# Performance work log

Hardware: AMD Instinct MI355X
Metric: run time of the kernel (lower is better)

## Reference

```python
import jax, jax.numpy as jnp
import numpy as np

DIM = 192
HEADS = 6
HIDDEN = 384  # int(DIM * 2.0)


def _ln(x, w, b):
    # WithBias LayerNorm over channel dim (torch normalizes last dim of b,(hw),c)
    mu = jnp.mean(x, axis=1, keepdims=True)
    var = jnp.var(x, axis=1, keepdims=True)
    return (x - mu) / jnp.sqrt(var + 1e-5) * w[None, :, None, None] + b[None, :, None, None]


def _conv1x1(x, w):  # w: [O, I, 1, 1]
    return jnp.einsum('bihw,oi->bohw', x, w[:, :, 0, 0])


def _dwconv3(x, w):  # depthwise 3x3, w: [C, 1, 3, 3]
    return jax.lax.conv_general_dilated(
        x, w, window_strides=(1, 1), padding=((1, 1), (1, 1)),
        feature_group_count=x.shape[1],
        dimension_numbers=('NCHW', 'OIHW', 'NCHW'))


def _l2norm(x):  # F.normalize along last axis
    n = jnp.sqrt(jnp.sum(x * x, axis=-1, keepdims=True))
    return x / jnp.maximum(n, 1e-12)


def setup_inputs() -> dict:
    key = jax.random.key(0)
    ks = jax.random.split(key, 16)
    s = 0.02
    d = {}
    d['x'] = jax.random.normal(ks[0], (2, DIM, 128, 128), dtype=jnp.float32)
    d['k_v'] = jax.random.normal(ks[1], (2, 256), dtype=jnp.float32)
    d['ln1_w'] = jnp.ones((DIM,), jnp.float32)
    d['ln1_b'] = jnp.zeros((DIM,), jnp.float32)
    d['temp'] = jnp.ones((HEADS, 1, 1), jnp.float32)
    d['w_kR'] = jax.random.normal(ks[2], (DIM * 3 // 4, 192), jnp.float32) * s
    d['w_kI'] = jax.random.normal(ks[3], (DIM // 4, 64), jnp.float32) * s
    d['w_qR'] = jax.random.normal(ks[4], (DIM, DIM * 3 // 4, 1, 1), jnp.float32) * s
    d['w_qdw'] = jax.random.normal(ks[5], (DIM, 1, 3, 3), jnp.float32) * s
    d['w_kvI'] = jax.random.normal(ks[6], (DIM * 2, DIM // 4, 1, 1), jnp.float32) * s
    d['w_kvdw'] = jax.random.normal(ks[7], (DIM * 2, 1, 3, 3), jnp.float32) * s
    d['w_po'] = jax.random.normal(ks[8], (DIM, DIM, 1, 1), jnp.float32) * s
    d['ln2_w'] = jnp.ones((DIM,), jnp.float32)
    d['ln2_b'] = jnp.zeros((DIM,), jnp.float32)
    d['w_ffk'] = jax.random.normal(ks[9], (DIM, 256), jnp.float32) * s
    d['w_pin'] = jax.random.normal(ks[10], (HIDDEN * 2, DIM, 1, 1), jnp.float32) * s
    d['w_dw'] = jax.random.normal(ks[11], (HIDDEN * 2, 1, 3, 3), jnp.float32) * s
    d['w_pout'] = jax.random.normal(ks[12], (DIM, HIDDEN, 1, 1), jnp.float32) * s
    return d


def reference(x, k_v, ln1_w, ln1_b, temp, w_kR, w_kI, w_qR, w_qdw, w_kvI, w_kvdw,
              w_po, ln2_w, ln2_b, w_ffk, w_pin, w_dw, w_pout):
    b, c, h, w = x.shape
    c3 = c * 3 // 4
    # ---- Rttention on norm1(x) ----
    xn = _ln(x, ln1_w, ln1_b)
    kvr = (k_v[:, :192] @ w_kR.T)[:, :, None, None]   # [b, 3c/4, 1, 1]
    kvi = (k_v[:, 192:] @ w_kI.T)[:, :, None, None]   # [b, c/4, 1, 1]
    x_r = xn[:, :c3] * kvr + xn[:, :c3]
    x_i = xn[:, c3:] * kvi + xn[:, c3:]
    q = _dwconv3(_conv1x1(x_r, w_qR), w_qdw)          # [b, c, h, w]
    kv = _dwconv3(_conv1x1(x_i, w_kvI), w_kvdw)       # [b, 2c, h, w]
    k, v = jnp.split(kv, 2, axis=1)
    rh = lambda t: t.reshape(b, HEADS, c // HEADS, h * w)
    q = _l2norm(rh(q))
    k = _l2norm(rh(k))
    v = rh(v)
    # channel-wise attention: [b, head, c_h, c_h]
    attn = jax.nn.softmax(jnp.einsum('bhcd,bhed->bhce', q, k) * temp[None], axis=-1)
    out = jnp.einsum('bhce,bhed->bhcd', attn, v).reshape(b, c, h, w)
    x = x + _conv1x1(out, w_po)
    # ---- GDFN FeedForward on norm2(x) ----
    xn2 = _ln(x, ln2_w, ln2_b)
    kvf = (k_v @ w_ffk.T)[:, :, None, None]           # [b, c, 1, 1]
    y = xn2 * kvf + xn2
    y = _dwconv3(_conv1x1(y, w_pin), w_dw)            # [b, 2*hidden, h, w]
    y1, y2 = jnp.split(y, 2, axis=1)
    y = jax.nn.gelu(y1, approximate=False) * y2
    x = x + _conv1x1(y, w_pout)
    return (x, k_v)
```

## Files before the change

### kernel.cpp

```cpp
#include <hip/hip_runtime.h>
#include <math.h>

#define HW 16384
#define IMG 128
#define CDIM 192
#define C3 144
#define C4 48
#define NB 2
#define NPX 32768
#define HEADS 6

typedef unsigned short u16;
typedef unsigned int u32;
typedef __attribute__((ext_vector_type(8))) short bf16x8;
typedef __attribute__((ext_vector_type(4))) float f32x4;

__device__ __forceinline__ float bf2f(u16 u) {
    return __uint_as_float(((unsigned int)u) << 16);
}
__device__ __forceinline__ u16 f2bf(float f) {
    unsigned int x = __float_as_uint(f);
    unsigned int r = x + 0x7fffu + ((x >> 16) & 1u);
    return (u16)(r >> 16);
}

static inline float* wsf(void* ws, size_t off) { return (float*)((char*)ws + off); }
static inline u16* wsh(void* ws, size_t off) { return (u16*)((char*)ws + off); }

__global__ void k_setup(const float* __restrict__ kvv, const float* __restrict__ wkR,
                        const float* __restrict__ wkI, const float* __restrict__ wffk,
                        const float* __restrict__ wqR, const float* __restrict__ wkvI,
                        const float* __restrict__ wpo, const float* __restrict__ wpin,
                        const float* __restrict__ wpout,
                        u16* __restrict__ wb, float* __restrict__ sm,
                        float* __restrict__ tail) {
    int t = blockIdx.x * 256 + threadIdx.x;
    if (t < 313344) {
        float v;
        if (t < 30720) {
            int o = t / 160, i = t % 160;
            v = (i < 144) ? wqR[o * 144 + i] : 0.f;
        } else if (t < 55296) {
            int r = t - 30720; int o = r / 64, i = r % 64;
            v = (i < 48) ? wkvI[o * 48 + i] : 0.f;
        } else if (t < 92160) {
            v = wpo[t - 55296];
        } else if (t < 239616) {
            v = wpin[t - 92160];
        } else {
            v = wpout[t - 239616];
        }
        wb[t] = f2bf(v);
    } else if (t < 314112) {
        int r = t - 313344;
        if (r < 288) {
            int b = r / 144, o = r % 144;
            const float* v = kvv + b * 256;
            const float* w = wkR + o * 192;
            float s = 0.f;
            for (int j = 0; j < 192; j++) s += v[j] * w[j];
            sm[r] = s + 1.0f;
        } else if (r < 384) {
            int r2 = r - 288;
            int b = r2 / 48, o = r2 % 48;
            const float* v = kvv + b * 256 + 192;
            const float* w = wkI + o * 64;
            float s = 0.f;
            for (int j = 0; j < 64; j++) s += v[j] * w[j];
            sm[288 + r2] = s + 1.0f;
        } else {
            int r2 = r - 384;
            int b = r2 / 192, o = r2 % 192;
            const float* v = kvv + b * 256;
            const float* w = wffk + o * 256;
            float s = 0.f;
            for (int j = 0; j < 256; j++) s += v[j] * w[j];
            sm[384 + r2] = s + 1.0f;
        }
    } else if (t < 314624) {
        int r = t - 314112;
        tail[r] = kvv[r];
    }
}

template <bool INBF, bool SPLIT>
__global__ __launch_bounds__(256) void k_ln(
    const void* __restrict__ xin,
    const float* __restrict__ lnw, const float* __restrict__ lnb,
    const float* __restrict__ sca, const float* __restrict__ scb,
    u16* __restrict__ outA, u16* __restrict__ outB) {
    __shared__ float red[2][16][16][4];
    __shared__ float mu_s[16][4], rstd_s[16][4];
    int t = threadIdx.x;
    int px4 = t & 15, cg = t >> 4;
    int base = blockIdx.x * 64;
    int b = base >> 14;
    int p = (base & 16383) + px4 * 4;
    float vals[12][4];
    float s[4] = {0.f, 0.f, 0.f, 0.f}, s2[4] = {0.f, 0.f, 0.f, 0.f};
#pragma unroll
    for (int j = 0; j < 12; j++) {
        int c = cg * 12 + j;
        size_t off = ((size_t)(b * CDIM + c)) * HW + p;
        float v[4];
        if (INBF) {
            ushort4 u = *(const ushort4*)((const u16*)xin + off);
            v[0] = bf2f(u.x); v[1] = bf2f(u.y); v[2] = bf2f(u.z); v[3] = bf2f(u.w);
        } else {
            float4 f = *(const float4*)((const float*)xin + off);
            v[0] = f.x; v[1] = f.y; v[2] = f.z; v[3] = f.w;
        }
#pragma unroll
        for (int q = 0; q < 4; q++) {
            vals[j][q] = v[q]; s[q] += v[q]; s2[q] += v[q] * v[q];
        }
    }
#pragma unroll
    for (int q = 0; q < 4; q++) { red[0][cg][px4][q] = s[q]; red[1][cg][px4][q] = s2[q]; }
    __syncthreads();
    if (t < 16) {
        float S[4] = {0.f, 0.f, 0.f, 0.f}, S2[4] = {0.f, 0.f, 0.f, 0.f};
        for (int g2 = 0; g2 < 16; g2++)
#pragma unroll
            for (int q = 0; q < 4; q++) { S[q] += red[0][g2][t][q]; S2[q] += red[1][g2][t][q]; }
#pragma unroll
        for (int q = 0; q < 4; q++) {
            float mu = S[q] * (1.0f / CDIM);
            float var = S2[q] * (1.0f / CDIM) - mu * mu;
            mu_s[t][q] = mu;
            rstd_s[t][q] = rsqrtf(var + 1e-5f);
        }
    }
    __syncthreads();
    float mu[4], rs[4];
#pragma unroll
    for (int q = 0; q < 4; q++) { mu[q] = mu_s[px4][q]; rs[q] = rstd_s[px4][q]; }
#pragma unroll
    for (int j = 0; j < 12; j++) {
        int c = cg * 12 + j;
        float w = lnw[c], bb = lnb[c];
        float sc; u16* op; size_t off;
        if (SPLIT) {
            if (c < C3) { sc = sca[b * C3 + c]; off = ((size_t)(b * C3 + c)) * HW + p; op = outA; }
            else { sc = scb[b * C4 + c - C3]; off = ((size_t)(b * C4 + c - C3)) * HW + p; op = outB; }
        } else {
            sc = sca[b * CDIM + c]; off = ((size_t)(b * CDIM + c)) * HW + p; op = outA;
        }
        ushort4 o;
        o.x = f2bf(((vals[j][0] - mu[0]) * rs[0] * w + bb) * sc);
        o.y = f2bf(((vals[j][1] - mu[1]) * rs[1] * w + bb) * sc);
        o.z = f2bf(((vals[j][2] - mu[2]) * rs[2] * w + bb) * sc);
        o.w = f2bf(((vals[j][3] - mu[3]) * rs[3] * w + bb) * sc);
        *(ushort4*)(op + off) = o;
    }
}

template <int NCH, int MODE>
__global__ __launch_bounds__(256) void k_gemm(
    const u16* __restrict__ X, int xrows,
    const u16* __restrict__ Wb,
    const void* __restrict__ resid, void* __restrict__ outp, int CO) {
    constexpr int CIP = NCH * 32;
    __shared__ __align__(16) u16 Ws[64 * 32];
    __shared__ __align__(16) u16 Xs[32 * 130];
    const int tid = threadIdx.x;
    const int n0 = blockIdx.x * 128;
    const int m0 = blockIdx.y * 64;
    const int b = blockIdx.z;
    const u16* Xb = X + (size_t)b * xrows * HW + n0;
    const int wave = tid >> 6, lane = tid & 63;
    const int quad = lane >> 4, l16 = lane & 15;
    const int smr = tid >> 2, sk4 = tid & 3;
    const int skr = tid >> 3, sc0 = (tid & 7) * 16;
    f32x4 acc[4][2] = {};
    for (int ch = 0; ch < NCH; ch++) {
        const int k0 = ch * 32;
        if (ch) __syncthreads();
        {
            const int4 wv = *(const int4*)(Wb + (size_t)(m0 + smr) * CIP + k0 + sk4 * 8);
            *(int4*)&Ws[(smr << 5) + (((sk4 ^ (smr & 3)) & 3) << 3)] = wv;
        }
        {
            const u16* xc = Xb + (size_t)(k0 + skr) * HW + sc0;
            int4 r0 = *(const int4*)xc;
            int4 r1 = *(const int4*)(xc + 8);
            u32* dst = (u32*)&Xs[skr * 130 + sc0];
#pragma unroll
            for (int i = 0; i < 4; i++) dst[i] = ((const u32*)&r0)[i];
#pragma unroll
            for (int i = 0; i < 4; i++) dst[4 + i] = ((const u32*)&r1)[i];
        }
        __syncthreads();
        bf16x8 af[4];
#pragma unroll
        for (int mi = 0; mi < 4; mi++) {
            int row = mi * 16 + l16;
            af[mi] = *(const bf16x8*)&Ws[(row << 5) + ((quad ^ (row & 3)) << 3)];
        }
#pragma unroll
        for (int ni = 0; ni < 2; ni++) {
            int n = wave * 32 + ni * 16 + l16;
            bf16x8 bfr;
#pragma unroll
            for (int j = 0; j < 8; j++) bfr[j] = (short)Xs[(quad * 8 + j) * 130 + n];
#pragma unroll
            for (int mi = 0; mi < 4; mi++)
                acc[mi][ni] = __builtin_amdgcn_mfma_f32_16x16x32_bf16(af[mi], bfr, acc[mi][ni], 0, 0, 0);
        }
    }
#pragma unroll
    for (int mi = 0; mi < 4; mi++) {
#pragma unroll
        for (int ni = 0; ni < 2; ni++) {
#pragma unroll
            for (int r = 0; r < 4; r++) {
                int m = m0 + mi * 16 + quad * 4 + r;
                int n = n0 + wave * 32 + ni * 16 + l16;
                size_t idx = ((size_t)b * CO + m) * HW + n;
                float v = acc[mi][ni][r];
                if (MODE == 0) {
                    ((u16*)outp)[idx] = f2bf(v);
                } else if (MODE == 1) {
                    v += ((const float*)resid)[idx];
                    ((u16*)outp)[idx] = f2bf(v);
                } else {
                    v += bf2f(((const u16*)resid)[idx]);
                    ((float*)outp)[idx] = v;
                }
            }
        }
    }
}

__global__ __launch_bounds__(256) void k_dw2(const u16* __restrict__ X,
                                             const float* __restrict__ Wd,
                                             u16* __restrict__ out, int C, int sqCh,
                                             float* __restrict__ sqp) {
    __shared__ float In[34 * 132];
    __shared__ float red[4];
    int bc = blockIdx.x >> 2, rt = blockIdx.x & 3;
    int b = bc / C, ch = bc % C;
    const u16* xb = X + (size_t)bc * HW;
    int t = threadIdx.x;
    int c0 = (t & 7) * 16;
    for (int r = t >> 3; r < 34; r += 32) {
        int y = rt * 32 - 1 + r;
        float* dst = &In[r * 132 + 1 + c0];
        if ((unsigned)y < 128u) {
            const u16* src = xb + y * 128 + c0;
            int4 r0 = *(const int4*)src;
            int4 r1 = *(const int4*)(src + 8);
            const u16* p0 = (const u16*)&r0;
            const u16* p1 = (const u16*)&r1;
#pragma unroll
            for (int i = 0; i < 8; i++) dst[i] = bf2f(p0[i]);
#pragma unroll
            for (int i = 0; i < 8; i++) dst[8 + i] = bf2f(p1[i]);
        } else {
#pragma unroll
            for (int i = 0; i < 16; i++) dst[i] = 0.f;
        }
    }
    if (t < 34) { In[t * 132] = 0.f; In[t * 132 + 129] = 0.f; }
    __syncthreads();
    const float* w = Wd + ch * 9;
    float w00 = w[0], w01 = w[1], w02 = w[2], w10 = w[3], w11 = w[4],
          w12 = w[5], w20 = w[6], w21 = w[7], w22 = w[8];
    int x = t & 127, rg = t >> 7;
    int base = rg * 16;
    float A2 = 0.f, A1 = 0.f, B1 = 0.f, ssq = 0.f;
    u16* ob = out + (size_t)bc * HW + (rt * 32 + base) * 128 + x;
#pragma unroll
    for (int r = 0; r < 18; r++) {
        const float* row = &In[(base + r) * 132 + x];
        float v0 = row[0], v1 = row[1], v2 = row[2];
        float h0 = w00 * v0 + w01 * v1 + w02 * v2;
        float h1 = w10 * v0 + w11 * v1 + w12 * v2;
        float h2 = w20 * v0 + w21 * v1 + w22 * v2;
        if (r >= 2) {
            float val = A2 + B1 + h2;
            ob[(size_t)(r - 2) * 128] = f2bf(val);
            ssq += val * val;
        }
        A2 = A1; A1 = h0; B1 = h1;
    }
    if (ch < sqCh) {
        for (int o = 32; o > 0; o >>= 1) ssq += __shfl_down(ssq, o, 64);
        int wid = t >> 6, lane = t & 63;
        if (lane == 0) red[wid] = ssq;
        __syncthreads();
        if (t == 0) sqp[((b * 192 + ch) << 2) | rt] = red[0] + red[1] + red[2] + red[3];
    }
}

__global__ __launch_bounds__(256) void k_dw_gelu2(const u16* __restrict__ G0,
                                                  const float* __restrict__ Wd,
                                                  u16* __restrict__ out) {
    __shared__ float In[2 * 34 * 132];
    int bc = blockIdx.x >> 2, rt = blockIdx.x & 3;
    int b = bc / 384, j = bc % 384;
    int t = threadIdx.x;
    int c0 = (t & 7) * 16;
    for (int pl = 0; pl < 2; pl++) {
        const u16* xb = G0 + ((size_t)b * 768 + pl * 384 + j) * HW;
        float* pla = &In[pl * 34 * 132];
        for (int r = t >> 3; r < 34; r += 32) {
            int y = rt * 32 - 1 + r;
            float* dst = &pla[r * 132 + 1 + c0];
            if ((unsigned)y < 128u) {
                const u16* src = xb + y * 128 + c0;
                int4 r0 = *(const int4*)src;
                int4 r1 = *(const int4*)(src + 8);
                const u16* p0 = (const u16*)&r0;
                const u16* p1 = (const u16*)&r1;
#pragma unroll
                for (int i = 0; i < 8; i++) dst[i] = bf2f(p0[i]);
#pragma unroll
                for (int i = 0; i < 8; i++) dst[8 + i] = bf2f(p1[i]);
            } else {
#pragma unroll
                for (int i = 0; i < 16; i++) dst[i] = 0.f;
            }
        }
        if (t < 34) { pla[t * 132] = 0.f; pla[t * 132 + 129] = 0.f; }
    }
    __syncthreads();
    const float* w1 = Wd + j * 9;
    const float* w2 = Wd + (384 + j) * 9;
    float a00 = w1[0], a01 = w1[1], a02 = w1[2], a10 = w1[3], a11 = w1[4],
          a12 = w1[5], a20 = w1[6], a21 = w1[7], a22 = w1[8];
    float b00 = w2[0], b01 = w2[1], b02 = w2[2], b10 = w2[3], b11 = w2[4],
          b12 = w2[5], b20 = w2[6], b21 = w2[7], b22 = w2[8];
    int x = t & 127, rg = t >> 7;
    int base = rg * 16;
    float A2a = 0.f, A1a = 0.f, B1a = 0.f;
    float A2b = 0.f, A1b = 0.f, B1b = 0.f;
    u16* ob = out + ((size_t)b * 384 + j) * HW + (rt * 32 + base) * 128 + x;
#pragma unroll
    for (int r = 0; r < 18; r++) {
        const float* r1p = &In[(base + r) * 132 + x];
        const float* r2p = r1p + 34 * 132;
        float u0 = r1p[0], u1 = r1p[1], u2 = r1p[2];
        float v0 = r2p[0], v1 = r2p[1], v2 = r2p[2];
        float h0a = a00 * u0 + a01 * u1 + a02 * u2;
        float h1a = a10 * u0 + a11 * u1 + a12 * u2;
        float h2a = a20 * u0 + a21 * u1 + a22 * u2;
        float h0b = b00 * v0 + b01 * v1 + b02 * v2;
        float h1b = b10 * v0 + b11 * v1 + b12 * v2;
        float h2b = b20 * v0 + b21 * v1 + b22 * v2;
        if (r >= 2) {
            float s1 = A2a + B1a + h2a;
            float s2 = A2b + B1b + h2b;
            float g = 0.5f * s1 * (1.0f + erff(s1 * 0.70710678118654752f));
            ob[(size_t)(r - 2) * 128] = f2bf(g * s2);
        }
        A2a = A1a; A1a = h0a; B1a = h1a;
        A2b = A1b; A1b = h0b; B1b = h1b;
    }
}

__global__ __launch_bounds__(256) void k_qk(const u16* __restrict__ qb_,
                                            const u16* __restrict__ kb_,
                                            float* __restrict__ Spart) {
    int bh = blockIdx.x >> 5, ds = blockIdx.x & 31;
    int b = bh / HEADS, h = bh % HEADS;
    int tid = threadIdx.x;
    int wave = tid >> 6, lane = tid & 63;
    int quad = lane >> 4, l16 = lane & 15;
    int tm = wave >> 1, tn = wave & 1;
    const u16* qrow = qb_ + ((size_t)(b * 192 + h * 32 + tm * 16 + l16)) * HW + ds * 512 + quad * 8;
    const u16* krow = kb_ + ((size_t)(b * 384 + h * 32 + tn * 16 + l16)) * HW + ds * 512 + quad * 8;
    f32x4 acc = {};
#pragma unroll
    for (int ch = 0; ch < 16; ch++) {
        bf16x8 a = *(const bf16x8*)(qrow + ch * 32);
        bf16x8 k8 = *(const bf16x8*)(krow + ch * 32);
        acc = __builtin_amdgcn_mfma_f32_16x16x32_bf16(a, k8, acc, 0, 0, 0);
    }
    float* Sb = Spart + ((size_t)ds * 12 + bh) * 1024;
#pragma unroll
    for (int r = 0; r < 4; r++)
        Sb[(tm * 16 + quad * 4 + r) * 32 + tn * 16 + l16] = acc[r];
}

__global__ void k_softmax(const float* __restrict__ Spart, const float* __restrict__ sqqp,
                          const float* __restrict__ sqkp, const float* __restrict__ temp,
                          u16* __restrict__ attnb) {
    int row = blockIdx.x;
    int bh = row >> 5, c2 = row & 31;
    int b = bh / HEADS, h = bh % HEADS;
    int e = threadIdx.x;
    float l = -1e30f;
    if (e < 32) {
        float s = 0.f;
        for (int d = 0; d < 32; d++) s += Spart[((size_t)d * 12 + bh) * 1024 + c2 * 32 + e];
        const float* qp = sqqp + (b * 192 + h * 32 + c2) * 4;
        const float* kp = sqkp + (b * 192 + h * 32 + e) * 4;
        float nq = qp[0] + qp[1] + qp[2] + qp[3];
        float nk = kp[0] + kp[1] + kp[2] + kp[3];
        float invq = 1.0f / fmaxf(sqrtf(nq), 1e-12f);
        float invk = 1.0f / fmaxf(sqrtf(nk), 1e-12f);
        l = s * invq * invk * temp[h];
    }
    float m = l;
    for (int o = 32; o > 0; o >>= 1) m = fmaxf(m, __shfl_xor(m, o, 64));
    float ev = (e < 32) ? expf(l - m) : 0.f;
    float ssum = ev;
    for (int o = 32; o > 0; o >>= 1) ssum += __shfl_xor(ssum, o, 64);
    if (e < 32) attnb[bh * 1024 + c2 * 32 + e] = f2bf(ev / ssum);
}

__global__ __launch_bounds__(256) void k_av(const u16* __restrict__ attnb,
                                            const u16* __restrict__ kvb,
                                            u16* __restrict__ out) {
    __shared__ __align__(16) u16 Vs[32 * 130];
    int bh = blockIdx.x >> 7;
    int pt = blockIdx.x & 127;
    int b = bh / HEADS, h = bh % HEADS;
    int p0 = pt * 128;
    int t = threadIdx.x;
    {
        int e = t >> 3, c0 = (t & 7) * 16;
        const u16* src = kvb + ((size_t)(b * 384 + 192 + h * 32 + e)) * HW + p0 + c0;
        int4 r0 = *(const int4*)src;
        int4 r1 = *(const int4*)(src + 8);
        u32* dst = (u32*)&Vs[e * 130 + c0];
#pragma unroll
        for (int i = 0; i < 4; i++) dst[i] = ((const u32*)&r0)[i];
#pragma unroll
        for (int i = 0; i < 4; i++) dst[4 + i] = ((const u32*)&r1)[i];
    }
    __syncthreads();
    int wave = t >> 6, lane = t & 63;
    int quad = lane >> 4, l16 = lane & 15;
    f32x4 acc[2][2] = {};
    bf16x8 af[2];
#pragma unroll
    for (int tm = 0; tm < 2; tm++)
        af[tm] = *(const bf16x8*)(attnb + bh * 1024 + (tm * 16 + l16) * 32 + quad * 8);
#pragma unroll
    for (int nt = 0; nt < 2; nt++) {
        int n = wave * 32 + nt * 16 + l16;
        bf16x8 bfr;
#pragma unroll
        for (int j = 0; j < 8; j++) bfr[j] = (short)Vs[(quad * 8 + j) * 130 + n];
#pragma unroll
        for (int tm = 0; tm < 2; tm++)
            acc[tm][nt] = __builtin_amdgcn_mfma_f32_16x16x32_bf16(af[tm], bfr, acc[tm][nt], 0, 0, 0);
    }
#pragma unroll
    for (int tm = 0; tm < 2; tm++)
#pragma unroll
        for (int nt = 0; nt < 2; nt++)
#pragma unroll
            for (int r = 0; r < 4; r++) {
                int c = h * 32 + tm * 16 + quad * 4 + r;
                int p = p0 + wave * 32 + nt * 16 + l16;
                out[((size_t)b * 192 + c) * HW + p] = f2bf(acc[tm][nt][r]);
            }
}

extern "C" void kernel_launch(void* const* d_in, const int* in_sizes, int n_in,
                              void* d_out, int out_size, void* d_ws, size_t ws_size,
                              hipStream_t stream) {
    const float* x     = (const float*)d_in[0];
    const float* k_v   = (const float*)d_in[1];
    const float* ln1w  = (const float*)d_in[2];
    const float* ln1b  = (const float*)d_in[3];
    const float* temp  = (const float*)d_in[4];
    const float* w_kR  = (const float*)d_in[5];
    const float* w_kI  = (const float*)d_in[6];
    const float* w_qR  = (const float*)d_in[7];
    const float* w_qdw = (const float*)d_in[8];
    const float* w_kvI = (const float*)d_in[9];
    const float* w_kvdw= (const float*)d_in[10];
    const float* w_po  = (const float*)d_in[11];
    const float* ln2w  = (const float*)d_in[12];
    const float* ln2b  = (const float*)d_in[13];
    const float* w_ffk = (const float*)d_in[14];
    const float* w_pin = (const float*)d_in[15];
    const float* w_dw  = (const float*)d_in[16];
    const float* w_pout= (const float*)d_in[17];
    float* out = (float*)d_out;

    const size_t MiB = 1048576ULL;
    u16*   q0b     = wsh(d_ws, 0);
    u16*   attnoutb= wsh(d_ws, 0);
    u16*   y0b     = wsh(d_ws, 0);
    u16*   kv0b    = wsh(d_ws, 12 * MiB);
    u16*   ybufb   = wsh(d_ws, 12 * MiB);
    u16*   x1b     = wsh(d_ws, 36 * MiB);
    u16*   qbuf_b  = wsh(d_ws, 48 * MiB);
    u16*   kvbuf_b = wsh(d_ws, 60 * MiB);
    u16*   xrb     = wsh(d_ws, 84 * MiB);
    u16*   xib     = wsh(d_ws, 94 * MiB);
    u16*   g0b     = wsh(d_ws, 98 * MiB);
    u16*   wb      = wsh(d_ws, 146 * MiB);
    float* sm      = wsf(d_ws, 147 * MiB);
    float* Spart   = wsf(d_ws, 148 * MiB);
    u16* wq   = wb;
    u16* wkv  = wb + 30720;
    u16* wpo  = wb + 55296;
    u16* wpin = wb + 92160;
    u16* wpout= wb + 239616;
    float* kvr  = sm;
    float* kvi  = sm + 288;
    float* kvf  = sm + 384;
    float* sqqp = sm + 768;
    float* sqkp = sm + 2304;
    u16*   attnb= (u16*)(sm + 3840);

    k_setup<<<1229, 256, 0, stream>>>(k_v, w_kR, w_kI, w_ffk, w_qR, w_kvI, w_po,
                                      w_pin, w_pout, wb, sm,
                                      out + (size_t)NB * CDIM * HW);
    k_ln<false, true><<<NPX / 64, 256, 0, stream>>>(x, ln1w, ln1b, kvr, kvi, xrb, xib);
    k_gemm<5, 0><<<dim3(128, 3, 2), 256, 0, stream>>>(xrb, 144, wq, nullptr, q0b, 192);
    k_gemm<2, 0><<<dim3(128, 6, 2), 256, 0, stream>>>(xib, 48, wkv, nullptr, kv0b, 384);
    k_dw2<<<NB * 192 * 4, 256, 0, stream>>>(q0b, w_qdw, qbuf_b, 192, 192, sqqp);
    k_dw2<<<NB * 384 * 4, 256, 0, stream>>>(kv0b, w_kvdw, kvbuf_b, 384, 192, sqkp);
    k_qk<<<12 * 32, 256, 0, stream>>>(qbuf_b, kvbuf_b, Spart);
    k_softmax<<<384, 64, 0, stream>>>(Spart, sqqp, sqkp, temp, attnb);
    k_av<<<12 * 128, 256, 0, stream>>>(attnb, kvbuf_b, attnoutb);
    k_gemm<6, 1><<<dim3(128, 3, 2), 256, 0, stream>>>(attnoutb, 192, wpo, x, x1b, 192);
    k_ln<true, false><<<NPX / 64, 256, 0, stream>>>(x1b, ln2w, ln2b, kvf, nullptr, y0b, nullptr);
    k_gemm<6, 0><<<dim3(128, 12, 2), 256, 0, stream>>>(y0b, 192, wpin, nullptr, g0b, 768);
    k_dw_gelu2<<<NB * 384 * 4, 256, 0, stream>>>(g0b, w_dw, ybufb);
    k_gemm<12, 2><<<dim3(128, 3, 2), 256, 0, stream>>>(ybufb, 384, wpout, x1b, out, 192);
}
```

Measured before the change: 268.6 us.

## Fold attention and LayerNorm2 into GEMM weights, merge q/kv kernels

```diff
diff --git a/kernel.cpp b/kernel.cpp
--- a/kernel.cpp
+++ b/kernel.cpp
@@ -80,15 +80,37 @@
     } else if (t < 314624) {
         int r = t - 314112;
         tail[r] = kvv[r];
-    }
-}
-
-template <bool INBF, bool SPLIT>
-__global__ __launch_bounds__(256) void k_ln(
-    const void* __restrict__ xin,
+    } else if (t < 326912) {
+        sm[3840 + (t - 314624)] = 0.f;
+    }
+}
+
+__global__ void k_setup2(const float* __restrict__ wpin, const float* __restrict__ lnw,
+                         const float* __restrict__ lnb, const float* __restrict__ kvf,
+                         u16* __restrict__ wpinb, float* __restrict__ rsum,
+                         float* __restrict__ biasp) {
+    int t = blockIdx.x * 256 + threadIdx.x;
+    if (t >= 1536) return;
+    int b = t / 768, m = t % 768;
+    float rs = 0.f, bi = 0.f;
+    u16* wrow = wpinb + (size_t)t * 192;
+    for (int c = 0; c < 192; c++) {
+        float w = wpin[m * 192 + c];
+        float s = kvf[b * 192 + c];
+        u16 h = f2bf(w * lnw[c] * s);
+        wrow[c] = h;
+        rs += bf2f(h);
+        bi += w * lnb[c] * s;
+    }
+    rsum[t] = rs;
+    biasp[t] = bi;
+}
+
+__global__ __launch_bounds__(256) void k_ln1(
+    const float* __restrict__ x,
     const float* __restrict__ lnw, const float* __restrict__ lnb,
     const float* __restrict__ sca, const float* __restrict__ scb,
-    u16* __restrict__ outA, u16* __restrict__ outB) {
+    u16* __restrict__ outA, u16* __restrict__ outB, u16* __restrict__ xb16) {
     __shared__ float red[2][16][16][4];
     __shared__ float mu_s[16][4], rstd_s[16][4];
     int t = threadIdx.x;
@@ -102,18 +124,13 @@
     for (int j = 0; j < 12; j++) {
         int c = cg * 12 + j;
         size_t off = ((size_t)(b * CDIM + c)) * HW + p;
-        float v[4];
-        if (INBF) {
-            ushort4 u = *(const ushort4*)((const u16*)xin + off);
-            v[0] = bf2f(u.x); v[1] = bf2f(u.y); v[2] = bf2f(u.z); v[3] = bf2f(u.w);
-        } else {
-            float4 f = *(const float4*)((const float*)xin + off);
-            v[0] = f.x; v[1] = f.y; v[2] = f.z; v[3] = f.w;
-        }
-#pragma unroll
-        for (int q = 0; q < 4; q++) {
-            vals[j][q] = v[q]; s[q] += v[q]; s2[q] += v[q] * v[q];
-        }
+        float4 f = *(const float4*)(x + off);
+        float v[4] = {f.x, f.y, f.z, f.w};
+        ushort4 o;
+        o.x = f2bf(v[0]); o.y = f2bf(v[1]); o.z = f2bf(v[2]); o.w = f2bf(v[3]);
+        *(ushort4*)(xb16 + off) = o;
+#pragma unroll
+        for (int q = 0; q < 4; q++) { vals[j][q] = v[q]; s[q] += v[q]; s2[q] += v[q] * v[q]; }
     }
 #pragma unroll
     for (int q = 0; q < 4; q++) { red[0][cg][px4][q] = s[q]; red[1][cg][px4][q] = s2[q]; }
@@ -140,12 +157,8 @@
         int c = cg * 12 + j;
         float w = lnw[c], bb = lnb[c];
         float sc; u16* op; size_t off;
-        if (SPLIT) {
-            if (c < C3) { sc = sca[b * C3 + c]; off = ((size_t)(b * C3 + c)) * HW + p; op = outA; }
-            else { sc = scb[b * C4 + c - C3]; off = ((size_t)(b * C4 + c - C3)) * HW + p; op = outB; }
-        } else {
-            sc = sca[b * CDIM + c]; off = ((size_t)(b * CDIM + c)) * HW + p; op = outA;
-        }
+        if (c < C3) { sc = sca[b * C3 + c]; off = ((size_t)(b * C3 + c)) * HW + p; op = outA; }
+        else { sc = scb[b * C4 + c - C3]; off = ((size_t)(b * C4 + c - C3)) * HW + p; op = outB; }
         ushort4 o;
         o.x = f2bf(((vals[j][0] - mu[0]) * rs[0] * w + bb) * sc);
         o.y = f2bf(((vals[j][1] - mu[1]) * rs[1] * w + bb) * sc);
@@ -155,29 +168,30 @@
     }
 }
 
-template <int NCH, int MODE>
-__global__ __launch_bounds__(256) void k_gemm(
-    const u16* __restrict__ X, int xrows,
-    const u16* __restrict__ Wb,
-    const void* __restrict__ resid, void* __restrict__ outp, int CO) {
-    constexpr int CIP = NCH * 32;
+__global__ __launch_bounds__(256) void k_gemm_qkv(
+    const u16* __restrict__ Xq, const u16* __restrict__ Xkv,
+    const u16* __restrict__ Wq, const u16* __restrict__ Wkv,
+    u16* __restrict__ Oq, u16* __restrict__ Okv) {
     __shared__ __align__(16) u16 Ws[64 * 32];
     __shared__ __align__(16) u16 Xs[32 * 130];
     const int tid = threadIdx.x;
     const int n0 = blockIdx.x * 128;
-    const int m0 = blockIdx.y * 64;
+    const int y = blockIdx.y;
     const int b = blockIdx.z;
+    const u16* X; const u16* Wb; u16* Op; int nch, cip, xrows, CO, m0;
+    if (y < 3) { X = Xq; Wb = Wq; Op = Oq; nch = 5; cip = 160; xrows = 144; CO = 192; m0 = y * 64; }
+    else { X = Xkv; Wb = Wkv; Op = Okv; nch = 2; cip = 64; xrows = 48; CO = 384; m0 = (y - 3) * 64; }
     const u16* Xb = X + (size_t)b * xrows * HW + n0;
     const int wave = tid >> 6, lane = tid & 63;
     const int quad = lane >> 4, l16 = lane & 15;
     const int smr = tid >> 2, sk4 = tid & 3;
     const int skr = tid >> 3, sc0 = (tid & 7) * 16;
     f32x4 acc[4][2] = {};
-    for (int ch = 0; ch < NCH; ch++) {
+    for (int ch = 0; ch < nch; ch++) {
         const int k0 = ch * 32;
         if (ch) __syncthreads();
         {
-            const int4 wv = *(const int4*)(Wb + (size_t)(m0 + smr) * CIP + k0 + sk4 * 8);
+            const int4 wv = *(const int4*)(Wb + (size_t)(m0 + smr) * cip + k0 + sk4 * 8);
             *(int4*)&Ws[(smr << 5) + (((sk4 ^ (smr & 3)) & 3) << 3)] = wv;
         }
         {
@@ -209,36 +223,30 @@
         }
     }
 #pragma unroll
-    for (int mi = 0; mi < 4; mi++) {
-#pragma unroll
-        for (int ni = 0; ni < 2; ni++) {
+    for (int mi = 0; mi < 4; mi++)
+#pragma unroll
+        for (int ni = 0; ni < 2; ni++)
 #pragma unroll
             for (int r = 0; r < 4; r++) {
                 int m = m0 + mi * 16 + quad * 4 + r;
                 int n = n0 + wave * 32 + ni * 16 + l16;
-                size_t idx = ((size_t)b * CO + m) * HW + n;
-                float v = acc[mi][ni][r];
-                if (MODE == 0) {
-                    ((u16*)outp)[idx] = f2bf(v);
-                } else if (MODE == 1) {
-                    v += ((const float*)resid)[idx];
-                    ((u16*)outp)[idx] = f2bf(v);
-                } else {
-                    v += bf2f(((const u16*)resid)[idx]);
-                    ((float*)outp)[idx] = v;
-                }
+                Op[((size_t)b * CO + m) * HW + n] = f2bf(acc[mi][ni][r]);
             }
-        }
-    }
-}
-
-__global__ __launch_bounds__(256) void k_dw2(const u16* __restrict__ X,
-                                             const float* __restrict__ Wd,
-                                             u16* __restrict__ out, int C, int sqCh,
-                                             float* __restrict__ sqp) {
+}
+
+__global__ __launch_bounds__(256) void k_dw2m(const u16* __restrict__ Xq,
+                                              const u16* __restrict__ Xkv,
+                                              const float* __restrict__ Wdq,
+                                              const float* __restrict__ Wdkv,
+                                              u16* __restrict__ outq, u16* __restrict__ outkv,
+                                              float* __restrict__ sqq, float* __restrict__ sqk) {
     __shared__ float In[34 * 132];
     __shared__ float red[4];
-    int bc = blockIdx.x >> 2, rt = blockIdx.x & 3;
+    int bid = blockIdx.x;
+    const u16* X; const float* Wd; u16* out; float* sqp; int C;
+    if (bid < 1536) { X = Xq; Wd = Wdq; out = outq; sqp = sqq; C = 192; }
+    else { bid -= 1536; X = Xkv; Wd = Wdkv; out = outkv; sqp = sqk; C = 384; }
+    int bc = bid >> 2, rt = bid & 3;
     int b = bc / C, ch = bc % C;
     const u16* xb = X + (size_t)bc * HW;
     int t = threadIdx.x;
@@ -284,12 +292,221 @@
         }
         A2 = A1; A1 = h0; B1 = h1;
     }
-    if (ch < sqCh) {
+    if (ch < 192) {
         for (int o = 32; o > 0; o >>= 1) ssq += __shfl_down(ssq, o, 64);
         int wid = t >> 6, lane = t & 63;
         if (lane == 0) red[wid] = ssq;
         __syncthreads();
         if (t == 0) sqp[((b * 192 + ch) << 2) | rt] = red[0] + red[1] + red[2] + red[3];
+    }
+}
+
+__global__ __launch_bounds__(256) void k_qk(const u16* __restrict__ qb_,
+                                            const u16* __restrict__ kb_,
+                                            float* __restrict__ S) {
+    int bh = blockIdx.x >> 5, ds = blockIdx.x & 31;
+    int b = bh / HEADS, h = bh % HEADS;
+    int tid = threadIdx.x;
+    int wave = tid >> 6, lane = tid & 63;
+    int quad = lane >> 4, l16 = lane & 15;
+    int tm = wave >> 1, tn = wave & 1;
+    const u16* qrow = qb_ + ((size_t)(b * 192 + h * 32 + tm * 16 + l16)) * HW + ds * 512 + quad * 8;
+    const u16* krow = kb_ + ((size_t)(b * 384 + h * 32 + tn * 16 + l16)) * HW + ds * 512 + quad * 8;
+    f32x4 acc = {};
+#pragma unroll
+    for (int ch = 0; ch < 16; ch++) {
+        bf16x8 a = *(const bf16x8*)(qrow + ch * 32);
+        bf16x8 k8 = *(const bf16x8*)(krow + ch * 32);
+        acc = __builtin_amdgcn_mfma_f32_16x16x32_bf16(a, k8, acc, 0, 0, 0);
+    }
+    float* Sb = S + bh * 1024;
+#pragma unroll
+    for (int r = 0; r < 4; r++)
+        atomicAdd(&Sb[(tm * 16 + quad * 4 + r) * 32 + tn * 16 + l16], acc[r]);
+}
+
+__global__ __launch_bounds__(256) void k_smA(const float* __restrict__ S,
+                                             const float* __restrict__ sqqp,
+                                             const float* __restrict__ sqkp,
+                                             const float* __restrict__ temp,
+                                             const float* __restrict__ wpo,
+                                             u16* __restrict__ weff) {
+    __shared__ float A[32][33];
+    __shared__ float scq[32], sck[32];
+    int bh = blockIdx.x;
+    int b = bh / HEADS, h = bh % HEADS;
+    int t = threadIdx.x;
+    if (t < 32) {
+        const float* qp = sqqp + (b * 192 + h * 32 + t) * 4;
+        const float* kp = sqkp + (b * 192 + h * 32 + t) * 4;
+        scq[t] = 1.0f / fmaxf(sqrtf(qp[0] + qp[1] + qp[2] + qp[3]), 1e-12f);
+        sck[t] = 1.0f / fmaxf(sqrtf(kp[0] + kp[1] + kp[2] + kp[3]), 1e-12f);
+    }
+    __syncthreads();
+    float tmp = temp[h];
+    for (int idx = t; idx < 1024; idx += 256) {
+        int r = idx >> 5, e = idx & 31;
+        A[r][e] = S[bh * 1024 + r * 32 + e] * scq[r] * sck[e] * tmp;
+    }
+    __syncthreads();
+    if (t < 32) {
+        float m = -1e30f;
+        for (int e = 0; e < 32; e++) m = fmaxf(m, A[t][e]);
+        float s = 0.f;
+        for (int e = 0; e < 32; e++) { float ev = expf(A[t][e] - m); A[t][e] = ev; s += ev; }
+        float inv = 1.0f / s;
+        for (int e = 0; e < 32; e++) A[t][e] *= inv;
+    }
+    __syncthreads();
+    for (int idx = t; idx < 6144; idx += 256) {
+        int m = idx >> 5, e = idx & 31;
+        float s = 0.f;
+        const float* wr = wpo + m * 192 + h * 32;
+#pragma unroll 8
+        for (int c = 0; c < 32; c++) s += wr[c] * A[c][e];
+        weff[((size_t)b * 192 + m) * 192 + h * 32 + e] = f2bf(s);
+    }
+}
+
+__global__ __launch_bounds__(256) void k_gemm_po(
+    const u16* __restrict__ kvb, const u16* __restrict__ weff,
+    const u16* __restrict__ residb, u16* __restrict__ outT,
+    float* __restrict__ sumP, float* __restrict__ sum2P) {
+    __shared__ __align__(16) u16 Ws[64 * 32];
+    __shared__ __align__(16) u16 Xs[32 * 130];
+    __shared__ __align__(16) u16 Lx[128 * 72];
+    const int tid = threadIdx.x;
+    const int n0 = blockIdx.x * 128;
+    const int m0 = blockIdx.y * 64;
+    const int b = blockIdx.z;
+    const u16* Xb = kvb + ((size_t)b * 384 + 192) * HW + n0;
+    const u16* Wb = weff + (size_t)b * 192 * 192;
+    const int wave = tid >> 6, lane = tid & 63;
+    const int quad = lane >> 4, l16 = lane & 15;
+    const int smr = tid >> 2, sk4 = tid & 3;
+    const int skr = tid >> 3, sc0 = (tid & 7) * 16;
+    f32x4 acc[4][2] = {};
+    for (int ch = 0; ch < 6; ch++) {
+        const int k0 = ch * 32;
+        if (ch) __syncthreads();
+        {
+            const int4 wv = *(const int4*)(Wb + (size_t)(m0 + smr) * 192 + k0 + sk4 * 8);
+            *(int4*)&Ws[(smr << 5) + (((sk4 ^ (smr & 3)) & 3) << 3)] = wv;
+        }
+        {
+            const u16* xc = Xb + (size_t)(k0 + skr) * HW + sc0;
+            int4 r0 = *(const int4*)xc;
+            int4 r1 = *(const int4*)(xc + 8);
+            u32* dst = (u32*)&Xs[skr * 130 + sc0];
+#pragma unroll
+            for (int i = 0; i < 4; i++) dst[i] = ((const u32*)&r0)[i];
+#pragma unroll
+            for (int i = 0; i < 4; i++) dst[4 + i] = ((const u32*)&r1)[i];
+        }
+        __syncthreads();
+        bf16x8 af[4];
+#pragma unroll
+        for (int mi = 0; mi < 4; mi++) {
+            int row = mi * 16 + l16;
+            af[mi] = *(const bf16x8*)&Ws[(row << 5) + ((quad ^ (row & 3)) << 3)];
+        }
+#pragma unroll
+        for (int ni = 0; ni < 2; ni++) {
+            int n = wave * 32 + ni * 16 + l16;
+            bf16x8 bfr;
+#pragma unroll
+            for (int j = 0; j < 8; j++) bfr[j] = (short)Xs[(quad * 8 + j) * 130 + n];
+#pragma unroll
+            for (int mi = 0; mi < 4; mi++)
+                acc[mi][ni] = __builtin_amdgcn_mfma_f32_16x16x32_bf16(af[mi], bfr, acc[mi][ni], 0, 0, 0);
+        }
+    }
+    float s1[2] = {0.f, 0.f}, s2[2] = {0.f, 0.f};
+#pragma unroll
+    for (int ni = 0; ni < 2; ni++) {
+        int nl = wave * 32 + ni * 16 + l16;
+#pragma unroll
+        for (int mi = 0; mi < 4; mi++)
+#pragma unroll
+            for (int r = 0; r < 4; r++) {
+                int mloc = mi * 16 + quad * 4 + r;
+                float v = acc[mi][ni][r] +
+                          bf2f(residb[((size_t)(b * 192 + m0 + mloc)) * HW + n0 + nl]);
+                s1[ni] += v; s2[ni] += v * v;
+                Lx[nl * 72 + mloc] = f2bf(v);
+            }
+        float a = s1[ni], c = s2[ni];
+        a += __shfl_xor(a, 16, 64); a += __shfl_xor(a, 32, 64);
+        c += __shfl_xor(c, 16, 64); c += __shfl_xor(c, 32, 64);
+        if (quad == 0) {
+            sumP[((size_t)(b * 3 + blockIdx.y)) * HW + n0 + nl] = a;
+            sum2P[((size_t)(b * 3 + blockIdx.y)) * HW + n0 + nl] = c;
+        }
+    }
+    __syncthreads();
+    {
+        int n = tid & 127, chunk = tid >> 7;
+        const int4* src = (const int4*)&Lx[n * 72 + chunk * 32];
+        int4 a0 = src[0], a1 = src[1], a2 = src[2], a3 = src[3];
+        int4* dst = (int4*)(outT + ((size_t)(b * 6 + (m0 >> 5) + chunk) * HW + n0 + n) * 32);
+        dst[0] = a0; dst[1] = a1; dst[2] = a2; dst[3] = a3;
+    }
+}
+
+__global__ __launch_bounds__(256) void k_pin(
+    const u16* __restrict__ xT, const u16* __restrict__ wpb,
+    const float* __restrict__ rsum, const float* __restrict__ biasp,
+    const float* __restrict__ sumP, const float* __restrict__ sum2P,
+    u16* __restrict__ out) {
+    const int tid = threadIdx.x;
+    const int n0 = blockIdx.x * 128;
+    const int m0 = blockIdx.y * 64;
+    const int b = blockIdx.z;
+    const int wave = tid >> 6, lane = tid & 63;
+    const int quad = lane >> 4, l16 = lane & 15;
+    const u16* wbase = wpb + ((size_t)(b * 768 + m0)) * 192;
+    f32x4 acc[4][2] = {};
+#pragma unroll
+    for (int ch = 0; ch < 6; ch++) {
+        bf16x8 af[4];
+#pragma unroll
+        for (int mi = 0; mi < 4; mi++)
+            af[mi] = *(const bf16x8*)(wbase + (size_t)(mi * 16 + l16) * 192 + ch * 32 + quad * 8);
+#pragma unroll
+        for (int ni = 0; ni < 2; ni++) {
+            bf16x8 bfr = *(const bf16x8*)(xT +
+                ((size_t)(b * 6 + ch) * HW + n0 + wave * 32 + ni * 16 + l16) * 32 + quad * 8);
+#pragma unroll
+            for (int mi = 0; mi < 4; mi++)
+                acc[mi][ni] = __builtin_amdgcn_mfma_f32_16x16x32_bf16(af[mi], bfr, acc[mi][ni], 0, 0, 0);
+        }
+    }
+    float rsv[4][4], biv[4][4];
+#pragma unroll
+    for (int mi = 0; mi < 4; mi++)
+#pragma unroll
+        for (int r = 0; r < 4; r++) {
+            int m = m0 + mi * 16 + quad * 4 + r;
+            rsv[mi][r] = rsum[b * 768 + m];
+            biv[mi][r] = biasp[b * 768 + m];
+        }
+#pragma unroll
+    for (int ni = 0; ni < 2; ni++) {
+        int n = n0 + wave * 32 + ni * 16 + l16;
+        size_t sb = (size_t)b * 3 * HW + n;
+        float P = sumP[sb] + sumP[sb + HW] + sumP[sb + 2 * HW];
+        float Q = sum2P[sb] + sum2P[sb + HW] + sum2P[sb + 2 * HW];
+        float mu = P * (1.0f / 192.0f);
+        float var = Q * (1.0f / 192.0f) - mu * mu;
+        float rstd = rsqrtf(var + 1e-5f);
+#pragma unroll
+        for (int mi = 0; mi < 4; mi++)
+#pragma unroll
+            for (int r = 0; r < 4; r++) {
+                int m = m0 + mi * 16 + quad * 4 + r;
+                float v = rstd * (acc[mi][ni][r] - mu * rsv[mi][r]) + biv[mi][r];
+                out[((size_t)(b * 768 + m)) * HW + n] = f2bf(v);
+            }
     }
 }
 
@@ -359,104 +576,67 @@
     }
 }
 
-__global__ __launch_bounds__(256) void k_qk(const u16* __restrict__ qb_,
-                                            const u16* __restrict__ kb_,
-                                            float* __restrict__ Spart) {
-    int bh = blockIdx.x >> 5, ds = blockIdx.x & 31;
-    int b = bh / HEADS, h = bh % HEADS;
-    int tid = threadIdx.x;
-    int wave = tid >> 6, lane = tid & 63;
-    int quad = lane >> 4, l16 = lane & 15;
-    int tm = wave >> 1, tn = wave & 1;
-    const u16* qrow = qb_ + ((size_t)(b * 192 + h * 32 + tm * 16 + l16)) * HW + ds * 512 + quad * 8;
-    const u16* krow = kb_ + ((size_t)(b * 384 + h * 32 + tn * 16 + l16)) * HW + ds * 512 + quad * 8;
-    f32x4 acc = {};
-#pragma unroll
-    for (int ch = 0; ch < 16; ch++) {
-        bf16x8 a = *(const bf16x8*)(qrow + ch * 32);
-        bf16x8 k8 = *(const bf16x8*)(krow + ch * 32);
-        acc = __builtin_amdgcn_mfma_f32_16x16x32_bf16(a, k8, acc, 0, 0, 0);
-    }
-    float* Sb = Spart + ((size_t)ds * 12 + bh) * 1024;
-#pragma unroll
-    for (int r = 0; r < 4; r++)
-        Sb[(tm * 16 + quad * 4 + r) * 32 + tn * 16 + l16] = acc[r];
-}
-
-__global__ void k_softmax(const float* __restrict__ Spart, const float* __restrict__ sqqp,
-                          const float* __restrict__ sqkp, const float* __restrict__ temp,
-                          u16* __restrict__ attnb) {
-    int row = blockIdx.x;
-    int bh = row >> 5, c2 = row & 31;
-    int b = bh / HEADS, h = bh % HEADS;
-    int e = threadIdx.x;
-    float l = -1e30f;
-    if (e < 32) {
-        float s = 0.f;
-        for (int d = 0; d < 32; d++) s += Spart[((size_t)d * 12 + bh) * 1024 + c2 * 32 + e];
-        const float* qp = sqqp + (b * 192 + h * 32 + c2) * 4;
-        const float* kp = sqkp + (b * 192 + h * 32 + e) * 4;
-        float nq = qp[0] + qp[1] + qp[2] + qp[3];
-        float nk = kp[0] + kp[1] + kp[2] + kp[3];
-        float invq = 1.0f / fmaxf(sqrtf(nq), 1e-12f);
-        float invk = 1.0f / fmaxf(sqrtf(nk), 1e-12f);
-        l = s * invq * invk * temp[h];
-    }
-    float m = l;
-    for (int o = 32; o > 0; o >>= 1) m = fmaxf(m, __shfl_xor(m, o, 64));
-    float ev = (e < 32) ? expf(l - m) : 0.f;
-    float ssum = ev;
-    for (int o = 32; o > 0; o >>= 1) ssum += __shfl_xor(ssum, o, 64);
-    if (e < 32) attnb[bh * 1024 + c2 * 32 + e] = f2bf(ev / ssum);
-}
-
-__global__ __launch_bounds__(256) void k_av(const u16* __restrict__ attnb,
-                                            const u16* __restrict__ kvb,
-                                            u16* __restrict__ out) {
-    __shared__ __align__(16) u16 Vs[32 * 130];
-    int bh = blockIdx.x >> 7;
-    int pt = blockIdx.x & 127;
-    int b = bh / HEADS, h = bh % HEADS;
-    int p0 = pt * 128;
-    int t = threadIdx.x;
-    {
-        int e = t >> 3, c0 = (t & 7) * 16;
-        const u16* src = kvb + ((size_t)(b * 384 + 192 + h * 32 + e)) * HW + p0 + c0;
-        int4 r0 = *(const int4*)src;
-        int4 r1 = *(const int4*)(src + 8);
-        u32* dst = (u32*)&Vs[e * 130 + c0];
-#pragma unroll
-        for (int i = 0; i < 4; i++) dst[i] = ((const u32*)&r0)[i];
-#pragma unroll
-        for (int i = 0; i < 4; i++) dst[4 + i] = ((const u32*)&r1)[i];
-    }
-    __syncthreads();
-    int wave = t >> 6, lane = t & 63;
-    int quad = lane >> 4, l16 = lane & 15;
-    f32x4 acc[2][2] = {};
-    bf16x8 af[2];
-#pragma unroll
-    for (int tm = 0; tm < 2; tm++)
-        af[tm] = *(const bf16x8*)(attnb + bh * 1024 + (tm * 16 + l16) * 32 + quad * 8);
-#pragma unroll
-    for (int nt = 0; nt < 2; nt++) {
-        int n = wave * 32 + nt * 16 + l16;
-        bf16x8 bfr;
-#pragma unroll
-        for (int j = 0; j < 8; j++) bfr[j] = (short)Vs[(quad * 8 + j) * 130 + n];
-#pragma unroll
-        for (int tm = 0; tm < 2; tm++)
-            acc[tm][nt] = __builtin_amdgcn_mfma_f32_16x16x32_bf16(af[tm], bfr, acc[tm][nt], 0, 0, 0);
-    }
-#pragma unroll
-    for (int tm = 0; tm < 2; tm++)
-#pragma unroll
-        for (int nt = 0; nt < 2; nt++)
+__global__ __launch_bounds__(256) void k_gemm_pout(
+    const u16* __restrict__ X, const u16* __restrict__ Wb,
+    const u16* __restrict__ residT, float* __restrict__ out) {
+    __shared__ __align__(16) u16 Ws[64 * 32];
+    __shared__ __align__(16) u16 Xs[32 * 130];
+    const int tid = threadIdx.x;
+    const int n0 = blockIdx.x * 128;
+    const int m0 = blockIdx.y * 64;
+    const int b = blockIdx.z;
+    const u16* Xb = X + (size_t)b * 384 * HW + n0;
+    const int wave = tid >> 6, lane = tid & 63;
+    const int quad = lane >> 4, l16 = lane & 15;
+    const int smr = tid >> 2, sk4 = tid & 3;
+    const int skr = tid >> 3, sc0 = (tid & 7) * 16;
+    f32x4 acc[4][2] = {};
+    for (int ch = 0; ch < 12; ch++) {
+        const int k0 = ch * 32;
+        if (ch) __syncthreads();
+        {
+            const int4 wv = *(const int4*)(Wb + (size_t)(m0 + smr) * 384 + k0 + sk4 * 8);
+            *(int4*)&Ws[(smr << 5) + (((sk4 ^ (smr & 3)) & 3) << 3)] = wv;
+        }
+        {
+            const u16* xc = Xb + (size_t)(k0 + skr) * HW + sc0;
+            int4 r0 = *(const int4*)xc;
+            int4 r1 = *(const int4*)(xc + 8);
+            u32* dst = (u32*)&Xs[skr * 130 + sc0];
+#pragma unroll
+            for (int i = 0; i < 4; i++) dst[i] = ((const u32*)&r0)[i];
+#pragma unroll
+            for (int i = 0; i < 4; i++) dst[4 + i] = ((const u32*)&r1)[i];
+        }
+        __syncthreads();
+        bf16x8 af[4];
+#pragma unroll
+        for (int mi = 0; mi < 4; mi++) {
+            int row = mi * 16 + l16;
+            af[mi] = *(const bf16x8*)&Ws[(row << 5) + ((quad ^ (row & 3)) << 3)];
+        }
+#pragma unroll
+        for (int ni = 0; ni < 2; ni++) {
+            int n = wave * 32 + ni * 16 + l16;
+            bf16x8 bfr;
+#pragma unroll
+            for (int j = 0; j < 8; j++) bfr[j] = (short)Xs[(quad * 8 + j) * 130 + n];
+#pragma unroll
+            for (int mi = 0; mi < 4; mi++)
+                acc[mi][ni] = __builtin_amdgcn_mfma_f32_16x16x32_bf16(af[mi], bfr, acc[mi][ni], 0, 0, 0);
+        }
+    }
+#pragma unroll
+    for (int mi = 0; mi < 4; mi++)
+#pragma unroll
+        for (int ni = 0; ni < 2; ni++)
 #pragma unroll
             for (int r = 0; r < 4; r++) {
-                int c = h * 32 + tm * 16 + quad * 4 + r;
-                int p = p0 + wave * 32 + nt * 16 + l16;
-                out[((size_t)b * 192 + c) * HW + p] = f2bf(acc[tm][nt][r]);
+                int m = m0 + mi * 16 + quad * 4 + r;
+                int n = n0 + wave * 32 + ni * 16 + l16;
+                float v = acc[mi][ni][r] +
+                          bf2f(residT[((size_t)(b * 6 + (m >> 5)) * HW + n) * 32 + (m & 31)]);
+                out[((size_t)(b * 192 + m)) * HW + n] = v;
             }
 }
 
@@ -485,45 +665,44 @@
 
     const size_t MiB = 1048576ULL;
     u16*   q0b     = wsh(d_ws, 0);
-    u16*   attnoutb= wsh(d_ws, 0);
-    u16*   y0b     = wsh(d_ws, 0);
-    u16*   kv0b    = wsh(d_ws, 12 * MiB);
-    u16*   ybufb   = wsh(d_ws, 12 * MiB);
-    u16*   x1b     = wsh(d_ws, 36 * MiB);
-    u16*   qbuf_b  = wsh(d_ws, 48 * MiB);
-    u16*   kvbuf_b = wsh(d_ws, 60 * MiB);
-    u16*   xrb     = wsh(d_ws, 84 * MiB);
-    u16*   xib     = wsh(d_ws, 94 * MiB);
-    u16*   g0b     = wsh(d_ws, 98 * MiB);
-    u16*   wb      = wsh(d_ws, 146 * MiB);
-    float* sm      = wsf(d_ws, 147 * MiB);
-    float* Spart   = wsf(d_ws, 148 * MiB);
+    u16*   kv0b    = wsh(d_ws, 16 * MiB);
+    u16*   qbuf_b  = wsh(d_ws, 40 * MiB);
+    u16*   kvbuf_b = wsh(d_ws, 56 * MiB);
+    u16*   xrb     = wsh(d_ws, 80 * MiB);
+    u16*   xib     = wsh(d_ws, 90 * MiB);
+    u16*   xb16    = wsh(d_ws, 94 * MiB);
+    u16*   x1T     = wsh(d_ws, 106 * MiB);
+    u16*   g0b     = wsh(d_ws, 118 * MiB);
+    u16*   ybufb   = wsh(d_ws, 166 * MiB);
+    u16*   wb      = wsh(d_ws, 190 * MiB);
+    u16*   weffb   = wsh(d_ws, 191 * MiB);
+    u16*   wpinb   = wsh(d_ws, 192 * MiB);
+    float* sm      = wsf(d_ws, 194 * MiB);
+    float* sumP    = wsf(d_ws, 196 * MiB);
+    float* sum2P   = wsf(d_ws, 197 * MiB);
     u16* wq   = wb;
     u16* wkv  = wb + 30720;
-    u16* wpo  = wb + 55296;
-    u16* wpin = wb + 92160;
     u16* wpout= wb + 239616;
     float* kvr  = sm;
     float* kvi  = sm + 288;
     float* kvf  = sm + 384;
     float* sqqp = sm + 768;
     float* sqkp = sm + 2304;
-    u16*   attnb= (u16*)(sm + 3840);
-
-    k_setup<<<1229, 256, 0, stream>>>(k_v, w_kR, w_kI, w_ffk, w_qR, w_kvI, w_po,
+    float* Smat = sm + 3840;
+    float* rsum = sm + 16128;
+    float* biasp= sm + 17664;
+
+    k_setup<<<1277, 256, 0, stream>>>(k_v, w_kR, w_kI, w_ffk, w_qR, w_kvI, w_po,
                                       w_pin, w_pout, wb, sm,
                                       out + (size_t)NB * CDIM * HW);
-    k_ln<false, true><<<NPX / 64, 256, 0, stream>>>(x, ln1w, ln1b, kvr, kvi, xrb, xib);
-    k_gemm<5, 0><<<dim3(128, 3, 2), 256, 0, stream>>>(xrb, 144, wq, nullptr, q0b, 192);
-    k_gemm<2, 0><<<dim3(128, 6, 2), 256, 0, stream>>>(xib, 48, wkv, nullptr, kv0b, 384);
-    k_dw2<<<NB * 192 * 4, 256, 0, stream>>>(q0b, w_qdw, qbuf_b, 192, 192, sqqp);
-    k_dw2<<<NB * 384 * 4, 256, 0, stream>>>(kv0b, w_kvdw, kvbuf_b, 384, 192, sqkp);
-    k_qk<<<12 * 32, 256, 0, stream>>>(qbuf_b, kvbuf_b, Spart);
-    k_softmax<<<384, 64, 0, stream>>>(Spart, sqqp, sqkp, temp, attnb);
-    k_av<<<12 * 128, 256, 0, stream>>>(attnb, kvbuf_b, attnoutb);
-    k_gemm<6, 1><<<dim3(128, 3, 2), 256, 0, stream>>>(attnoutb, 192, wpo, x, x1b, 192);
-    k_ln<true, false><<<NPX / 64, 256, 0, stream>>>(x1b, ln2w, ln2b, kvf, nullptr, y0b, nullptr);
-    k_gemm<6, 0><<<dim3(128, 12, 2), 256, 0, stream>>>(y0b, 192, wpin, nullptr, g0b, 768);
+    k_setup2<<<6, 256, 0, stream>>>(w_pin, ln2w, ln2b, kvf, wpinb, rsum, biasp);
+    k_ln1<<<NPX / 64, 256, 0, stream>>>(x, ln1w, ln1b, kvr, kvi, xrb, xib, xb16);
+    k_gemm_qkv<<<dim3(128, 9, 2), 256, 0, stream>>>(xrb, xib, wq, wkv, q0b, kv0b);
+    k_dw2m<<<4608, 256, 0, stream>>>(q0b, kv0b, w_qdw, w_kvdw, qbuf_b, kvbuf_b, sqqp, sqkp);
+    k_qk<<<12 * 32, 256, 0, stream>>>(qbuf_b, kvbuf_b, Smat);
+    k_smA<<<12, 256, 0, stream>>>(Smat, sqqp, sqkp, temp, w_po, weffb);
+    k_gemm_po<<<dim3(128, 3, 2), 256, 0, stream>>>(kvbuf_b, weffb, xb16, x1T, sumP, sum2P);
+    k_pin<<<dim3(128, 12, 2), 256, 0, stream>>>(x1T, wpinb, rsum, biasp, sumP, sum2P, g0b);
     k_dw_gelu2<<<NB * 384 * 4, 256, 0, stream>>>(g0b, w_dw, ybufb);
-    k_gemm<12, 2><<<dim3(128, 3, 2), 256, 0, stream>>>(ybufb, 384, wpout, x1b, out, 192);
-}
+    k_gemm_pout<<<dim3(128, 3, 2), 256, 0, stream>>>(ybufb, wpout, x1T, out);
+}
```

Result: slower. 306.8 us (+14.3%).
